# Kernel tuning notes

Measured on AMD Instinct MI355X. Metric: run time of the kernel, lower is better.

The kernel has to match this reference:

```python
import jax, jax.numpy as jnp
import numpy as np

DIM = 768
NUM_HEADS = 12
HEAD_DIM = DIM // NUM_HEADS
H = W = 64
RANK = 4
LORA_SCALING = 1.0 / RANK  # lora_alpha(=1) / r


def setup_inputs() -> dict:
    key = jax.random.key(0)
    ks = jax.random.split(key, 11)
    s = 0.02
    return {
        "x": jax.random.normal(ks[0], (1, H, W, DIM), dtype=jnp.float32),
        "W_qkv": jax.random.normal(ks[1], (3 * DIM, DIM), dtype=jnp.float32) * s,
        "b_qkv": jax.random.normal(ks[2], (3 * DIM,), dtype=jnp.float32) * s,
        "A_q": jax.random.normal(ks[3], (RANK, DIM), dtype=jnp.float32) * s,
        "B_q": jax.random.normal(ks[4], (DIM, RANK), dtype=jnp.float32) * s,
        "A_v": jax.random.normal(ks[5], (RANK, DIM), dtype=jnp.float32) * s,
        "B_v": jax.random.normal(ks[6], (DIM, RANK), dtype=jnp.float32) * s,
        "rel_h": jax.random.normal(ks[7], (2 * H - 1, HEAD_DIM), dtype=jnp.float32) * s,
        "rel_w": jax.random.normal(ks[8], (2 * W - 1, HEAD_DIM), dtype=jnp.float32) * s,
        "W_proj": jax.random.normal(ks[9], (DIM, DIM), dtype=jnp.float32) * s,
        "b_proj": jax.random.normal(ks[10], (DIM,), dtype=jnp.float32) * s,
    }


def _get_rel_pos(size, rel_pos):
    # q_size == k_size == size; relative coords indexed into (2*size-1, head_dim)
    coords = jnp.arange(size)[:, None] - jnp.arange(size)[None, :] + (size - 1)
    return rel_pos[coords]  # (size, size, head_dim)


def reference(x, W_qkv, b_qkv, A_q, B_q, A_v, B_v, rel_h, rel_w, W_proj, b_proj):
    B, h, w, dim = x.shape
    nh, hd = NUM_HEADS, HEAD_DIM
    scale = hd ** -0.5
    n = h * w
    xf = x.reshape(B, n, dim)

    # LoRA-merged QKV: base linear + low-rank deltas on q and v thirds only
    qkv = xf @ W_qkv.T + b_qkv  # (B, n, 3*dim)
    dq = ((xf @ A_q.T) @ B_q.T) * LORA_SCALING
    dv = ((xf @ A_v.T) @ B_v.T) * LORA_SCALING
    qkv = qkv.at[..., :dim].add(dq).at[..., 2 * dim:].add(dv)

    qkv = qkv.reshape(B, n, 3, nh, hd).transpose(2, 0, 3, 1, 4).reshape(3, B * nh, n, hd)
    q, k, v = qkv[0], qkv[1], qkv[2]  # each (B*nh, n, hd)

    attn = (q * scale) @ jnp.swapaxes(k, -2, -1)  # (B*nh, n, n)

    # decomposed relative position bias (SAM style)
    Rh = _get_rel_pos(h, rel_h)  # (h, h, hd)
    Rw = _get_rel_pos(w, rel_w)  # (w, w, hd)
    r_q = q.reshape(B * nh, h, w, hd)
    bias_h = jnp.einsum("bhwc,hkc->bhwk", r_q, Rh)  # (B*nh, h, w, h)
    bias_w = jnp.einsum("bhwc,wkc->bhwk", r_q, Rw)  # (B*nh, h, w, w)
    attn = (attn.reshape(B * nh, h, w, h, w)
            + bias_h[:, :, :, :, None]
            + bias_w[:, :, :, None, :]).reshape(B * nh, n, n)

    attn = jax.nn.softmax(attn, axis=-1)
    out = (attn @ v).reshape(B, nh, h, w, hd).transpose(0, 2, 3, 1, 4).reshape(B, h, w, dim)
    return out @ W_proj.T + b_proj
```

## Files before the change

### kernel.cpp

```cpp
#include <hip/hip_runtime.h>

#define NTOK 4096
#define DIMD 768
#define NHD  12
#define HDD  64

typedef float  f32x4  __attribute__((ext_vector_type(4)));
typedef float  f32x16 __attribute__((ext_vector_type(16)));
typedef short  s16x8  __attribute__((ext_vector_type(8)));

#define MFMA16(a, b, c) __builtin_amdgcn_mfma_f32_16x16x32_bf16(a, b, c, 0, 0, 0)
#define MFMA32(a, b, c) __builtin_amdgcn_mfma_f32_32x32x16_bf16(a, b, c, 0, 0, 0)

__device__ inline short f2b(float f) {
  unsigned u = __float_as_uint(f);
  u += 0x7FFFu + ((u >> 16) & 1u);
  return (short)(u >> 16);
}
__device__ inline float b2f(short s) {
  return __uint_as_float(((unsigned)(unsigned short)s) << 16);
}
__device__ inline void gl_lds16(const short* g, short* l) {
  __builtin_amdgcn_global_load_lds(
      (const __attribute__((address_space(1))) unsigned int*)g,
      (__attribute__((address_space(3))) unsigned int*)l, 16, 0, 0);
}


#define N_WQ  1769472
#define N_WP  589824
__global__ __launch_bounds__(256)
void k_conv(const float* __restrict__ wq, const float* __restrict__ wp,
            short* __restrict__ wqb, short* __restrict__ wpb) {
  long e = (long)(blockIdx.x * 256 + threadIdx.x) * 4;
  const float* src; short* dst;
  if (e < N_WQ) { src = wq + e; dst = wqb + e; }
  else { src = wp + (e - N_WQ); dst = wpb + (e - N_WQ); }
  float4 v = *(const float4*)src;
  short4 b; b.x = f2b(v.x); b.y = f2b(v.y); b.z = f2b(v.z); b.w = f2b(v.w);
  *(short4*)dst = b;
}

__global__ __launch_bounds__(64)
void k_lora(const float* __restrict__ x, const float* __restrict__ Aq,
            const float* __restrict__ Av, float* __restrict__ xaq,
            float* __restrict__ xav, short* __restrict__ xb) {
  const int i = blockIdx.x;
  const int l = threadIdx.x;
  float xv[12];
#pragma unroll
  for (int k = 0; k < 12; ++k) xv[k] = x[i * DIMD + l + 64 * k];
#pragma unroll
  for (int k = 0; k < 12; ++k) xb[i * DIMD + l + 64 * k] = f2b(xv[k]);
#pragma unroll
  for (int o = 0; o < 8; ++o) {
    const float* A = (o < 4) ? (Aq + o * DIMD) : (Av + (o - 4) * DIMD);
    float acc = 0.f;
#pragma unroll
    for (int k = 0; k < 12; ++k) acc = fmaf(xv[k], A[l + 64 * k], acc);
#pragma unroll
    for (int off = 32; off; off >>= 1) acc += __shfl_xor(acc, off, 64);
    if (l == o) {
      if (o < 4) xaq[i * 4 + o] = acc;
      else       xav[i * 4 + (o - 4)] = acc;
    }
  }
}

__global__ __launch_bounds__(256)
void k_qkv(const short* __restrict__ xb, const short* __restrict__ wb,
           const float* __restrict__ bqkv, const float* __restrict__ Bq,
           const float* __restrict__ Bv, const float* __restrict__ xaq,
           const float* __restrict__ xav, short* __restrict__ qkvb) {
  const int j0 = blockIdx.x * 128;
  const int i0 = blockIdx.y * 128;
  __shared__ short As[128 * 32];
  __shared__ short Bs[128 * 32];
  const int t = threadIdx.x, lane = t & 63, w = t >> 6;
  const int l15 = lane & 15, quad = lane >> 4;
  const int wm = w >> 1, wn = w & 1;

  f32x4 acc[4][4];
#pragma unroll
  for (int a = 0; a < 4; ++a)
#pragma unroll
    for (int b = 0; b < 4; ++b) acc[a][b] = (f32x4){0.f, 0.f, 0.f, 0.f};

  for (int kk = 0; kk < DIMD; kk += 32) {
    __syncthreads();
#pragma unroll
    for (int rep = 0; rep < 2; ++rep) {
      int c = rep * 256 + w * 64 + lane;
      gl_lds16(xb + (size_t)(i0 + (c >> 2)) * DIMD + kk + (c & 3) * 8,
               &As[(rep * 256 + w * 64) * 8]);
      gl_lds16(wb + (size_t)(j0 + (c >> 2)) * DIMD + kk + (c & 3) * 8,
               &Bs[(rep * 256 + w * 64) * 8]);
    }
    __syncthreads();
    s16x8 af[4], bf[4];
#pragma unroll
    for (int mt = 0; mt < 4; ++mt)
      af[mt] = *(const s16x8*)&As[(wm * 64 + mt * 16 + l15) * 32 + quad * 8];
#pragma unroll
    for (int nt = 0; nt < 4; ++nt)
      bf[nt] = *(const s16x8*)&Bs[(wn * 64 + nt * 16 + l15) * 32 + quad * 8];
#pragma unroll
    for (int mt = 0; mt < 4; ++mt)
#pragma unroll
      for (int nt = 0; nt < 4; ++nt)
        acc[mt][nt] = MFMA16(af[mt], bf[nt], acc[mt][nt]);
  }

  const int which = j0 / DIMD;
  float bj[4]; int jj[4], head[4], dd[4];
#pragma unroll
  for (int nt = 0; nt < 4; ++nt) {
    int j = j0 + wn * 64 + nt * 16 + l15;
    bj[nt] = bqkv[j];
    jj[nt] = j - which * DIMD;
    head[nt] = jj[nt] >> 6;
    dd[nt] = jj[nt] & 63;
  }
#pragma unroll
  for (int mt = 0; mt < 4; ++mt)
#pragma unroll
    for (int r = 0; r < 4; ++r) {
      const int i = i0 + wm * 64 + mt * 16 + quad * 4 + r;
      float aq0 = 0, aq1 = 0, aq2 = 0, aq3 = 0;
      if (which == 0) {
        const float* a = xaq + i * 4;
        aq0 = a[0]; aq1 = a[1]; aq2 = a[2]; aq3 = a[3];
      } else if (which == 2) {
        const float* a = xav + i * 4;
        aq0 = a[0]; aq1 = a[1]; aq2 = a[2]; aq3 = a[3];
      }
#pragma unroll
      for (int nt = 0; nt < 4; ++nt) {
        float v = acc[mt][nt][r] + bj[nt];
        if (which == 0) {
          const float* B = Bq + jj[nt] * 4;
          v += 0.25f * (aq0 * B[0] + aq1 * B[1] + aq2 * B[2] + aq3 * B[3]);
        } else if (which == 2) {
          const float* B = Bv + jj[nt] * 4;
          v += 0.25f * (aq0 * B[0] + aq1 * B[1] + aq2 * B[2] + aq3 * B[3]);
        }
        qkvb[(((size_t)which * NHD + head[nt]) * NTOK + i) * HDD + dd[nt]] = f2b(v);
      }
    }
}

__global__ __launch_bounds__(256)
void k_vt(const short* __restrict__ qkvb, short* __restrict__ vtb) {
  const int head = blockIdx.y;
  const int n0 = blockIdx.x * 64;
  const short* vg = qkvb + ((size_t)(2 * NHD + head)) * NTOK * HDD;
  __shared__ short T[64][68];
  const int t = threadIdx.x;
#pragma unroll
  for (int rp = 0; rp < 4; ++rp) {
    int f = t + 256 * rp;
    int n = f >> 4, c4 = (f & 15) * 4;
    *(short4*)&T[n][c4] = *(const short4*)&vg[(size_t)(n0 + n) * HDD + c4];
  }
  __syncthreads();
#pragma unroll
  for (int rp = 0; rp < 4; ++rp) {
    int f = t + 256 * rp;
    int d = f >> 4, n4 = (f & 15) * 4;
    short4 o;
    o.x = T[n4 + 0][d]; o.y = T[n4 + 1][d];
    o.z = T[n4 + 2][d]; o.w = T[n4 + 3][d];
    *(short4*)&vtb[((size_t)head * HDD + d) * NTOK + n0 + n4] = o;
  }
}

__global__ __launch_bounds__(256)
void k_attn3(const short* __restrict__ qkvb, const short* __restrict__ vtb,
             const float* __restrict__ relh, const float* __restrict__ relw,
             short* __restrict__ attnb) {
  const int head = blockIdx.y;
  const int hq = blockIdx.x;
  const int n0 = hq * 64;

  __shared__ short sm[17664];
  short* Ks   = sm;
  short* Vt   = sm + 4608;
  short* bHb  = sm + 9216;
  short* tbuf = sm + 13312;
  float* psb  = (float*)(sm + 17536);
  float* obuf = (float*)sm;

  const short* qg  = qkvb + (size_t)(0 * NHD + head) * NTOK * HDD;
  const short* kg  = qkvb + (size_t)(1 * NHD + head) * NTOK * HDD;
  const short* vtg = vtb + (size_t)head * HDD * NTOK;

  const int t = threadIdx.x;
  const int w = t >> 6, lane = t & 63;
  const int l31 = lane & 31, h = lane >> 5;
  const int kh = w >> 1, qh = w & 1;
  const int q = qh * 32 + l31;

  const int sa0 = t >> 3, sc0 = (t & 7) * 8, sa1 = sa0 + 32;

  s16x8 kr0 = *(const s16x8*)&kg[(size_t)sa0 * HDD + sc0];
  s16x8 kr1 = *(const s16x8*)&kg[(size_t)sa1 * HDD + sc0];
  s16x8 vr0 = *(const s16x8*)&vtg[(size_t)sa0 * NTOK + sc0];
  s16x8 vr1 = *(const s16x8*)&vtg[(size_t)sa1 * NTOK + sc0];

  s16x8 qb[4];
#pragma unroll
  for (int s = 0; s < 4; ++s)
    qb[s] = *(const s16x8*)&qg[(size_t)(n0 + q) * HDD + s * 16 + 8 * h];

#pragma unroll
  for (int rp = 0; rp < 4; ++rp) {
    int f = t + 256 * rp;
    int d = f >> 3, c = (f & 7) * 8;
    float4 v0 = make_float4(0, 0, 0, 0), v1 = v0;
    if (d < 127) {
      const float* s_ = relw + (size_t)d * HDD + c;
      v0 = *(const float4*)s_; v1 = *(const float4*)(s_ + 4);
    }
    short4 b0, b1;
    b0.x = f2b(v0.x); b0.y = f2b(v0.y); b0.z = f2b(v0.z); b0.w = f2b(v0.w);
    b1.x = f2b(v1.x); b1.y = f2b(v1.y); b1.z = f2b(v1.z); b1.w = f2b(v1.w);
    *(short4*)&sm[d * 72 + c] = b0;
    *(short4*)&sm[d * 72 + c + 4] = b1;
  }
  __syncthreads();

  f32x16 mc0 = (f32x16)(0.f), mc1 = (f32x16)(0.f);
#pragma unroll
  for (int s = 0; s < 4; ++s) {
    s16x8 a0 = *(const s16x8*)&sm[((kh * 2) * 32 + l31) * 72 + s * 16 + 8 * h];
    s16x8 a1 = *(const s16x8*)&sm[((kh * 2 + 1) * 32 + l31) * 72 + s * 16 + 8 * h];
    mc0 = MFMA32(a0, qb[s], mc0);
    mc1 = MFMA32(a1, qb[s], mc1);
  }
  __syncthreads();
#pragma unroll
  for (int reg = 0; reg < 16; ++reg) {
    int dl = (reg & 3) + 8 * (reg >> 2) + 4 * h;
    sm[(kh * 64 + dl) * 64 + q] = f2b(mc0[reg]);
    sm[(kh * 64 + 32 + dl) * 64 + q] = f2b(mc1[reg]);
  }
  __syncthreads();

  float bwl2[16];
#pragma unroll
  for (int reg = 0; reg < 16; ++reg) {
    int kl64 = kh * 32 + (reg & 3) + 8 * (reg >> 2) + 4 * h;
    int dneed = q - kl64 + 63;
    bwl2[reg] = b2f(sm[dneed * 64 + q]) * 1.44269504f;
  }
  __syncthreads();

#pragma unroll
  for (int rp = 0; rp < 2; ++rp) {
    int f = t + 256 * rp;
    int kt = f >> 3, c = (f & 7) * 8;
    const float* s_ = relh + (size_t)(hq + 63 - kt) * HDD + c;
    float4 v0 = *(const float4*)s_, v1 = *(const float4*)(s_ + 4);
    short4 b0, b1;
    b0.x = f2b(v0.x); b0.y = f2b(v0.y); b0.z = f2b(v0.z); b0.w = f2b(v0.w);
    b1.x = f2b(v1.x); b1.y = f2b(v1.y); b1.z = f2b(v1.z); b1.w = f2b(v1.w);
    *(short4*)&Vt[kt * 72 + c] = b0;
    *(short4*)&Vt[kt * 72 + c + 4] = b1;
  }
  __syncthreads();

  f32x16 hc = (f32x16)(0.f);
#pragma unroll
  for (int s = 0; s < 4; ++s) {
    s16x8 a = *(const s16x8*)&Vt[(kh * 32 + l31) * 72 + s * 16 + 8 * h];
    hc = MFMA32(a, qb[s], hc);
  }
#pragma unroll
  for (int reg = 0; reg < 16; ++reg) {
    int ktl = kh * 32 + (reg & 3) + 8 * (reg >> 2) + 4 * h;
    bHb[ktl * 64 + q] = f2b(hc[reg]);
  }

  float ps = 0.f;
  f32x16 oc0 = (f32x16)(0.f), oc1 = (f32x16)(0.f);

  for (int kt = 0; kt < 64; ++kt) {
    __syncthreads();
    *(s16x8*)&Ks[sa0 * 72 + sc0] = kr0;
    *(s16x8*)&Ks[sa1 * 72 + sc0] = kr1;
    *(s16x8*)&Vt[sa0 * 72 + sc0] = vr0;
    *(s16x8*)&Vt[sa1 * 72 + sc0] = vr1;
    __syncthreads();
    if (kt < 63) {
      const int nk = (kt + 1) * 64;
      kr0 = *(const s16x8*)&kg[(size_t)(nk + sa0) * HDD + sc0];
      kr1 = *(const s16x8*)&kg[(size_t)(nk + sa1) * HDD + sc0];
      vr0 = *(const s16x8*)&vtg[(size_t)sa0 * NTOK + nk + sc0];
      vr1 = *(const s16x8*)&vtg[(size_t)sa1 * NTOK + nk + sc0];
    }

    f32x16 sc_ = (f32x16)(0.f);
#pragma unroll
    for (int s = 0; s < 4; ++s) {
      s16x8 a = *(const s16x8*)&Ks[(kh * 32 + l31) * 72 + s * 16 + 8 * h];
      sc_ = MFMA32(a, qb[s], sc_);
    }

    float bhl2 = b2f(bHb[kt * 64 + q]) * 1.44269504f;
    float sv[16];
#pragma unroll
    for (int reg = 0; reg < 16; ++reg)
      sv[reg] = exp2f(fmaf(0.18033688f, sc_[reg], bhl2 + bwl2[reg]));
#pragma unroll
    for (int reg = 0; reg < 16; ++reg) ps += sv[reg];

    unsigned pk[8], sw[8];
#pragma unroll
    for (int i = 0; i < 8; ++i) {
      int rl = 4 * (i >> 1) + 2 * (i & 1);
      unsigned lo = __float_as_uint(sv[rl]) >> 16;
      unsigned hi = __float_as_uint(sv[rl + 1]) & 0xFFFF0000u;
      pk[i] = hi | lo;
    }
#pragma unroll
    for (int i = 0; i < 8; ++i)
      sw[i] = (unsigned)__shfl_xor((int)pk[i], 32, 64);

#pragma unroll
    for (int s2 = 0; s2 < 2; ++s2) {
      union { unsigned u[4]; s16x8 v; } B;
      B.u[0] = h ? sw[4 * s2 + 2] : pk[4 * s2 + 0];
      B.u[1] = h ? sw[4 * s2 + 3] : pk[4 * s2 + 1];
      B.u[2] = h ? pk[4 * s2 + 2] : sw[4 * s2 + 0];
      B.u[3] = h ? pk[4 * s2 + 3] : sw[4 * s2 + 1];
      s16x8 a0 = *(const s16x8*)&Vt[l31 * 72 + kh * 32 + s2 * 16 + 8 * h];
      s16x8 a1 = *(const s16x8*)&Vt[(32 + l31) * 72 + kh * 32 + s2 * 16 + 8 * h];
      oc0 = MFMA32(a0, B.v, oc0);
      oc1 = MFMA32(a1, B.v, oc1);
    }
  }

  __syncthreads();
  ps += __shfl_xor(ps, 32, 64);
  if (kh == 1) {
#pragma unroll
    for (int reg = 0; reg < 16; ++reg) {
      int dl = (reg & 3) + 8 * (reg >> 2) + 4 * h;
      obuf[dl * 66 + q] = oc0[reg];
      obuf[(32 + dl) * 66 + q] = oc1[reg];
    }
    if (lane < 32) psb[q] = ps;
  }
  __syncthreads();
  if (kh == 0) {
    float inv = 1.f / (ps + psb[q]);
#pragma unroll
    for (int reg = 0; reg < 16; ++reg) {
      int dl = (reg & 3) + 8 * (reg >> 2) + 4 * h;
      tbuf[dl * 66 + q] = f2b((oc0[reg] + obuf[dl * 66 + q]) * inv);
      tbuf[(32 + dl) * 66 + q] = f2b((oc1[reg] + obuf[(32 + dl) * 66 + q]) * inv);
    }
  }
  __syncthreads();
  {
    int qq = t >> 2, seg = t & 3;
    unsigned wds[8];
#pragma unroll
    for (int m = 0; m < 8; ++m) {
      unsigned lo = (unsigned short)tbuf[(seg * 16 + 2 * m) * 66 + qq];
      unsigned hi = (unsigned short)tbuf[(seg * 16 + 2 * m + 1) * 66 + qq];
      wds[m] = lo | (hi << 16);
    }
    short* dst = attnb + (size_t)(n0 + qq) * DIMD + head * 64 + seg * 16;
    *(int4*)dst = *(int4*)&wds[0];
    *(int4*)(dst + 8) = *(int4*)&wds[4];
  }
}

__global__ __launch_bounds__(256)
void k_proj(const short* __restrict__ ab, const short* __restrict__ wpb,
            const float* __restrict__ bp, float* __restrict__ out) {
  const int j0 = blockIdx.x * 64;
  const int i0 = blockIdx.y * 128;
  __shared__ short As[128 * 32];
  __shared__ short Bs[64 * 32];
  const int t = threadIdx.x, lane = t & 63, w = t >> 6;
  const int l15 = lane & 15, quad = lane >> 4;
  const int wm = w >> 1, wn = w & 1;

  f32x4 acc[4][2];
#pragma unroll
  for (int a = 0; a < 4; ++a)
#pragma unroll
    for (int b = 0; b < 2; ++b) acc[a][b] = (f32x4){0.f, 0.f, 0.f, 0.f};

  for (int kk = 0; kk < DIMD; kk += 32) {
    __syncthreads();
#pragma unroll
    for (int rep = 0; rep < 2; ++rep) {
      int c = rep * 256 + w * 64 + lane;
      gl_lds16(ab + (size_t)(i0 + (c >> 2)) * DIMD + kk + (c & 3) * 8,
               &As[(rep * 256 + w * 64) * 8]);
    }
    {
      gl_lds16(wpb + (size_t)(j0 + ((w * 64 + lane) >> 2)) * DIMD + kk +
                   ((w * 64 + lane) & 3) * 8,
               &Bs[(w * 64) * 8]);
    }
    __syncthreads();
    s16x8 af[4], bf[2];
#pragma unroll
    for (int mt = 0; mt < 4; ++mt)
      af[mt] = *(const s16x8*)&As[(wm * 64 + mt * 16 + l15) * 32 + quad * 8];
#pragma unroll
    for (int nt = 0; nt < 2; ++nt)
      bf[nt] = *(const s16x8*)&Bs[(wn * 32 + nt * 16 + l15) * 32 + quad * 8];
#pragma unroll
    for (int mt = 0; mt < 4; ++mt)
#pragma unroll
      for (int nt = 0; nt < 2; ++nt)
        acc[mt][nt] = MFMA16(af[mt], bf[nt], acc[mt][nt]);
  }

#pragma unroll
  for (int mt = 0; mt < 4; ++mt)
#pragma unroll
    for (int r = 0; r < 4; ++r) {
      const int i = i0 + wm * 64 + mt * 16 + quad * 4 + r;
#pragma unroll
      for (int nt = 0; nt < 2; ++nt) {
        const int j = j0 + wn * 32 + nt * 16 + l15;
        out[(size_t)i * DIMD + j] = acc[mt][nt][r] + bp[j];
      }
    }
}

extern "C" void kernel_launch(void* const* d_in, const int* in_sizes, int n_in,
                              void* d_out, int out_size, void* d_ws, size_t ws_size,
                              hipStream_t stream) {
  (void)in_sizes; (void)n_in; (void)out_size; (void)ws_size;
  const float* x    = (const float*)d_in[0];
  const float* Wqkv = (const float*)d_in[1];
  const float* bqkv = (const float*)d_in[2];
  const float* Aq   = (const float*)d_in[3];
  const float* Bq   = (const float*)d_in[4];
  const float* Av   = (const float*)d_in[5];
  const float* Bv   = (const float*)d_in[6];
  const float* relh = (const float*)d_in[7];
  const float* relw = (const float*)d_in[8];
  const float* Wp   = (const float*)d_in[9];
  const float* bp   = (const float*)d_in[10];
  float* out = (float*)d_out;

  float* ws = (float*)d_ws;
  float* xaq  = ws;
  float* xav  = ws + 16384;
  short* xb    = (short*)(ws + 32768);
  short* wqkvb = (short*)(ws + 1605632);
  short* wpb   = (short*)(ws + 2490368);
  short* qkvb  = (short*)(ws + 2785280);
  short* vtb   = (short*)(ws + 7503872);
  short* attnb = (short*)(ws + 9076736);

  k_conv<<<dim3(2304), dim3(256), 0, stream>>>(Wqkv, Wp, wqkvb, wpb);
  k_lora<<<dim3(NTOK), dim3(64), 0, stream>>>(x, Aq, Av, xaq, xav, xb);
  k_qkv<<<dim3(18, 32), dim3(256), 0, stream>>>(xb, wqkvb, bqkv, Bq, Bv, xaq,
                                                xav, qkvb);
  k_vt<<<dim3(64, NHD), dim3(256), 0, stream>>>(qkvb, vtb);
  k_attn3<<<dim3(64, NHD), dim3(256), 0, stream>>>(qkvb, vtb, relh, relw, attnb);
  k_proj<<<dim3(12, 32), dim3(256), 0, stream>>>(attnb, wpb, bp, out);
}
```

Baseline: 262.7 us.

## Fold LoRA into QKV GEMM K-dim and double-buffer attention K/V via LDS DMA

The LoRA low-rank terms are folded into the QKV GEMM by extending the reduction dimension from 768 to 800. The extra columns hold x·A scaled by 1/4 on the activation side and B on the weight side, which removes the per-element LoRA epilogue and the separate xaq/xav buffers. The attention kernel now streams K and V^T tiles straight into double-buffered, XOR-swizzled LDS with global_load_lds instead of staging them through registers, so there is one barrier per iteration instead of two. Weight conversion is merged into one prep kernel. Costs are about 4% more GEMM work and bf16 rounding of the LoRA factors.

```diff
diff --git a/kernel.cpp b/kernel.cpp
--- a/kernel.cpp
+++ b/kernel.cpp
@@ -4,6 +4,7 @@
 #define DIMD 768
 #define NHD  12
 #define HDD  64
+#define DK   800
 
 typedef float  f32x4  __attribute__((ext_vector_type(4)));
 typedef float  f32x16 __attribute__((ext_vector_type(16)));
@@ -27,31 +28,47 @@
 }
 
 
-#define N_WQ  1769472
-#define N_WP  589824
-__global__ __launch_bounds__(256)
-void k_conv(const float* __restrict__ wq, const float* __restrict__ wp,
-            short* __restrict__ wqb, short* __restrict__ wpb) {
-  long e = (long)(blockIdx.x * 256 + threadIdx.x) * 4;
-  const float* src; short* dst;
-  if (e < N_WQ) { src = wq + e; dst = wqb + e; }
-  else { src = wp + (e - N_WQ); dst = wpb + (e - N_WQ); }
-  float4 v = *(const float4*)src;
-  short4 b; b.x = f2b(v.x); b.y = f2b(v.y); b.z = f2b(v.z); b.w = f2b(v.w);
-  *(short4*)dst = b;
-}
-
 __global__ __launch_bounds__(64)
-void k_lora(const float* __restrict__ x, const float* __restrict__ Aq,
-            const float* __restrict__ Av, float* __restrict__ xaq,
-            float* __restrict__ xav, short* __restrict__ xb) {
+void k_prep_w(const float* __restrict__ Wqkv, const float* __restrict__ Bq,
+              const float* __restrict__ Bv, const float* __restrict__ Wp,
+              short* __restrict__ we, short* __restrict__ wpb) {
+  const int j = blockIdx.x;
+  const int l = threadIdx.x;
+  if (j < 2304) {
+#pragma unroll
+    for (int k = 0; k < 12; ++k)
+      we[(size_t)j * DK + l + 64 * k] = f2b(Wqkv[(size_t)j * DIMD + l + 64 * k]);
+    if (l < 32) {
+      int c = 768 + l;
+      short v = 0;
+      if (l < 4) {
+        if (j < 768) v = f2b(Bq[j * 4 + l]);
+      } else if (l < 8) {
+        if (j >= 1536) v = f2b(Bv[(j - 1536) * 4 + (l - 4)]);
+      }
+      we[(size_t)j * DK + c] = v;
+    }
+  } else {
+    const int jr = j - 2304;
+#pragma unroll
+    for (int k = 0; k < 12; ++k)
+      wpb[(size_t)jr * DIMD + l + 64 * k] =
+          f2b(Wp[(size_t)jr * DIMD + l + 64 * k]);
+  }
+}
+
+__global__ __launch_bounds__(64)
+void k_prep_x(const float* __restrict__ x, const float* __restrict__ Aq,
+              const float* __restrict__ Av, short* __restrict__ xe) {
   const int i = blockIdx.x;
   const int l = threadIdx.x;
   float xv[12];
 #pragma unroll
-  for (int k = 0; k < 12; ++k) xv[k] = x[i * DIMD + l + 64 * k];
-#pragma unroll
-  for (int k = 0; k < 12; ++k) xb[i * DIMD + l + 64 * k] = f2b(xv[k]);
+  for (int k = 0; k < 12; ++k) xv[k] = x[(size_t)i * DIMD + l + 64 * k];
+#pragma unroll
+  for (int k = 0; k < 12; ++k)
+    xe[(size_t)i * DK + l + 64 * k] = f2b(xv[k]);
+  float a8[8];
 #pragma unroll
   for (int o = 0; o < 8; ++o) {
     const float* A = (o < 4) ? (Aq + o * DIMD) : (Av + (o - 4) * DIMD);
@@ -60,18 +77,20 @@
     for (int k = 0; k < 12; ++k) acc = fmaf(xv[k], A[l + 64 * k], acc);
 #pragma unroll
     for (int off = 32; off; off >>= 1) acc += __shfl_xor(acc, off, 64);
-    if (l == o) {
-      if (o < 4) xaq[i * 4 + o] = acc;
-      else       xav[i * 4 + (o - 4)] = acc;
-    }
+    a8[o] = acc;
+  }
+  if (l < 32) {
+    float v = 0.f;
+#pragma unroll
+    for (int o = 0; o < 8; ++o)
+      if (l == o) v = 0.25f * a8[o];
+    xe[(size_t)i * DK + 768 + l] = (l < 8) ? f2b(v) : (short)0;
   }
 }
 
 __global__ __launch_bounds__(256)
-void k_qkv(const short* __restrict__ xb, const short* __restrict__ wb,
-           const float* __restrict__ bqkv, const float* __restrict__ Bq,
-           const float* __restrict__ Bv, const float* __restrict__ xaq,
-           const float* __restrict__ xav, short* __restrict__ qkvb) {
+void k_qkv(const short* __restrict__ xe, const short* __restrict__ we,
+           const float* __restrict__ bqkv, short* __restrict__ qkvb) {
   const int j0 = blockIdx.x * 128;
   const int i0 = blockIdx.y * 128;
   __shared__ short As[128 * 32];
@@ -86,14 +105,14 @@
 #pragma unroll
     for (int b = 0; b < 4; ++b) acc[a][b] = (f32x4){0.f, 0.f, 0.f, 0.f};
 
-  for (int kk = 0; kk < DIMD; kk += 32) {
+  for (int kk = 0; kk < DK; kk += 32) {
     __syncthreads();
 #pragma unroll
     for (int rep = 0; rep < 2; ++rep) {
       int c = rep * 256 + w * 64 + lane;
-      gl_lds16(xb + (size_t)(i0 + (c >> 2)) * DIMD + kk + (c & 3) * 8,
+      gl_lds16(xe + (size_t)(i0 + (c >> 2)) * DK + kk + (c & 3) * 8,
                &As[(rep * 256 + w * 64) * 8]);
-      gl_lds16(wb + (size_t)(j0 + (c >> 2)) * DIMD + kk + (c & 3) * 8,
+      gl_lds16(we + (size_t)(j0 + (c >> 2)) * DK + kk + (c & 3) * 8,
                &Bs[(rep * 256 + w * 64) * 8]);
     }
     __syncthreads();
@@ -112,40 +131,24 @@
   }
 
   const int which = j0 / DIMD;
-  float bj[4]; int jj[4], head[4], dd[4];
+  float bj[4]; int head[4], dd[4];
 #pragma unroll
   for (int nt = 0; nt < 4; ++nt) {
     int j = j0 + wn * 64 + nt * 16 + l15;
     bj[nt] = bqkv[j];
-    jj[nt] = j - which * DIMD;
-    head[nt] = jj[nt] >> 6;
-    dd[nt] = jj[nt] & 63;
+    int jj = j - which * DIMD;
+    head[nt] = jj >> 6;
+    dd[nt] = jj & 63;
   }
 #pragma unroll
   for (int mt = 0; mt < 4; ++mt)
 #pragma unroll
     for (int r = 0; r < 4; ++r) {
       const int i = i0 + wm * 64 + mt * 16 + quad * 4 + r;
-      float aq0 = 0, aq1 = 0, aq2 = 0, aq3 = 0;
-      if (which == 0) {
-        const float* a = xaq + i * 4;
-        aq0 = a[0]; aq1 = a[1]; aq2 = a[2]; aq3 = a[3];
-      } else if (which == 2) {
-        const float* a = xav + i * 4;
-        aq0 = a[0]; aq1 = a[1]; aq2 = a[2]; aq3 = a[3];
-      }
-#pragma unroll
-      for (int nt = 0; nt < 4; ++nt) {
-        float v = acc[mt][nt][r] + bj[nt];
-        if (which == 0) {
-          const float* B = Bq + jj[nt] * 4;
-          v += 0.25f * (aq0 * B[0] + aq1 * B[1] + aq2 * B[2] + aq3 * B[3]);
-        } else if (which == 2) {
-          const float* B = Bv + jj[nt] * 4;
-          v += 0.25f * (aq0 * B[0] + aq1 * B[1] + aq2 * B[2] + aq3 * B[3]);
-        }
-        qkvb[(((size_t)which * NHD + head[nt]) * NTOK + i) * HDD + dd[nt]] = f2b(v);
-      }
+#pragma unroll
+      for (int nt = 0; nt < 4; ++nt)
+        qkvb[(((size_t)which * NHD + head[nt]) * NTOK + i) * HDD + dd[nt]] =
+            f2b(acc[mt][nt][r] + bj[nt]);
     }
 }
 
@@ -175,20 +178,15 @@
 }
 
 __global__ __launch_bounds__(256)
-void k_attn3(const short* __restrict__ qkvb, const short* __restrict__ vtb,
+void k_attn4(const short* __restrict__ qkvb, const short* __restrict__ vtb,
              const float* __restrict__ relh, const float* __restrict__ relw,
              short* __restrict__ attnb) {
   const int head = blockIdx.y;
   const int hq = blockIdx.x;
   const int n0 = hq * 64;
 
-  __shared__ short sm[17664];
-  short* Ks   = sm;
-  short* Vt   = sm + 4608;
-  short* bHb  = sm + 9216;
-  short* tbuf = sm + 13312;
-  float* psb  = (float*)(sm + 17536);
-  float* obuf = (float*)sm;
+  __shared__ short sm[20480];
+  short* smb = sm;
 
   const short* qg  = qkvb + (size_t)(0 * NHD + head) * NTOK * HDD;
   const short* kg  = qkvb + (size_t)(1 * NHD + head) * NTOK * HDD;
@@ -200,12 +198,13 @@
   const int kh = w >> 1, qh = w & 1;
   const int q = qh * 32 + l31;
 
-  const int sa0 = t >> 3, sc0 = (t & 7) * 8, sa1 = sa0 + 32;
-
-  s16x8 kr0 = *(const s16x8*)&kg[(size_t)sa0 * HDD + sc0];
-  s16x8 kr1 = *(const s16x8*)&kg[(size_t)sa1 * HDD + sc0];
-  s16x8 vr0 = *(const s16x8*)&vtg[(size_t)sa0 * NTOK + sc0];
-  s16x8 vr1 = *(const s16x8*)&vtg[(size_t)sa1 * NTOK + sc0];
+  const int slot = w * 64 + lane;
+  const int krow = slot >> 3;
+  const int kcol = ((slot & 7) ^ (krow & 7)) * 8;
+  const short* gK0 = kg + (size_t)krow * HDD + kcol;
+  const short* gK1 = gK0 + 32 * HDD;
+  const short* gV0 = vtg + (size_t)krow * NTOK + kcol;
+  const short* gV1 = gV0 + (size_t)32 * NTOK;
 
   s16x8 qb[4];
 #pragma unroll
@@ -224,16 +223,16 @@
     short4 b0, b1;
     b0.x = f2b(v0.x); b0.y = f2b(v0.y); b0.z = f2b(v0.z); b0.w = f2b(v0.w);
     b1.x = f2b(v1.x); b1.y = f2b(v1.y); b1.z = f2b(v1.z); b1.w = f2b(v1.w);
-    *(short4*)&sm[d * 72 + c] = b0;
-    *(short4*)&sm[d * 72 + c + 4] = b1;
+    *(short4*)&smb[d * 72 + c] = b0;
+    *(short4*)&smb[d * 72 + c + 4] = b1;
   }
   __syncthreads();
 
   f32x16 mc0 = (f32x16)(0.f), mc1 = (f32x16)(0.f);
 #pragma unroll
   for (int s = 0; s < 4; ++s) {
-    s16x8 a0 = *(const s16x8*)&sm[((kh * 2) * 32 + l31) * 72 + s * 16 + 8 * h];
-    s16x8 a1 = *(const s16x8*)&sm[((kh * 2 + 1) * 32 + l31) * 72 + s * 16 + 8 * h];
+    s16x8 a0 = *(const s16x8*)&smb[((kh * 2) * 32 + l31) * 72 + s * 16 + 8 * h];
+    s16x8 a1 = *(const s16x8*)&smb[((kh * 2 + 1) * 32 + l31) * 72 + s * 16 + 8 * h];
     mc0 = MFMA32(a0, qb[s], mc0);
     mc1 = MFMA32(a1, qb[s], mc1);
   }
@@ -241,8 +240,8 @@
 #pragma unroll
   for (int reg = 0; reg < 16; ++reg) {
     int dl = (reg & 3) + 8 * (reg >> 2) + 4 * h;
-    sm[(kh * 64 + dl) * 64 + q] = f2b(mc0[reg]);
-    sm[(kh * 64 + 32 + dl) * 64 + q] = f2b(mc1[reg]);
+    smb[(kh * 64 + dl) * 64 + q] = f2b(mc0[reg]);
+    smb[(kh * 64 + 32 + dl) * 64 + q] = f2b(mc1[reg]);
   }
   __syncthreads();
 
@@ -251,7 +250,7 @@
   for (int reg = 0; reg < 16; ++reg) {
     int kl64 = kh * 32 + (reg & 3) + 8 * (reg >> 2) + 4 * h;
     int dneed = q - kl64 + 63;
-    bwl2[reg] = b2f(sm[dneed * 64 + q]) * 1.44269504f;
+    bwl2[reg] = b2f(smb[dneed * 64 + q]) * 1.44269504f;
   }
   __syncthreads();
 
@@ -264,83 +263,93 @@
     short4 b0, b1;
     b0.x = f2b(v0.x); b0.y = f2b(v0.y); b0.z = f2b(v0.z); b0.w = f2b(v0.w);
     b1.x = f2b(v1.x); b1.y = f2b(v1.y); b1.z = f2b(v1.z); b1.w = f2b(v1.w);
-    *(short4*)&Vt[kt * 72 + c] = b0;
-    *(short4*)&Vt[kt * 72 + c + 4] = b1;
+    *(short4*)&smb[kt * 72 + c] = b0;
+    *(short4*)&smb[kt * 72 + c + 4] = b1;
   }
   __syncthreads();
 
   f32x16 hc = (f32x16)(0.f);
 #pragma unroll
   for (int s = 0; s < 4; ++s) {
-    s16x8 a = *(const s16x8*)&Vt[(kh * 32 + l31) * 72 + s * 16 + 8 * h];
+    s16x8 a = *(const s16x8*)&smb[(kh * 32 + l31) * 72 + s * 16 + 8 * h];
     hc = MFMA32(a, qb[s], hc);
   }
 #pragma unroll
   for (int reg = 0; reg < 16; ++reg) {
     int ktl = kh * 32 + (reg & 3) + 8 * (reg >> 2) + 4 * h;
-    bHb[ktl * 64 + q] = f2b(hc[reg]);
-  }
+    smb[16384 + ktl * 64 + q] = f2b(hc[reg]);
+  }
+  __syncthreads();
+
+  gl_lds16(gK0, smb + 0 + w * 512);
+  gl_lds16(gK1, smb + 2048 + w * 512);
+  gl_lds16(gV0, smb + 8192 + w * 512);
+  gl_lds16(gV1, smb + 8192 + 2048 + w * 512);
+  gK0 += 4096; gK1 += 4096; gV0 += 64; gV1 += 64;
+
+  int baseS[4], baseV[2];
+#pragma unroll
+  for (int s = 0; s < 4; ++s)
+    baseS[s] = (kh * 32 + l31) * 64 + (((2 * s + h) ^ (l31 & 7)) * 8);
+#pragma unroll
+  for (int s2 = 0; s2 < 2; ++s2)
+    baseV[s2] = l31 * 64 + (((kh * 4 + s2 * 2 + h) ^ (l31 & 7)) * 8);
 
   float ps = 0.f;
   f32x16 oc0 = (f32x16)(0.f), oc1 = (f32x16)(0.f);
 
-  for (int kt = 0; kt < 64; ++kt) {
-    __syncthreads();
-    *(s16x8*)&Ks[sa0 * 72 + sc0] = kr0;
-    *(s16x8*)&Ks[sa1 * 72 + sc0] = kr1;
-    *(s16x8*)&Vt[sa0 * 72 + sc0] = vr0;
-    *(s16x8*)&Vt[sa1 * 72 + sc0] = vr1;
-    __syncthreads();
-    if (kt < 63) {
-      const int nk = (kt + 1) * 64;
-      kr0 = *(const s16x8*)&kg[(size_t)(nk + sa0) * HDD + sc0];
-      kr1 = *(const s16x8*)&kg[(size_t)(nk + sa1) * HDD + sc0];
-      vr0 = *(const s16x8*)&vtg[(size_t)sa0 * NTOK + nk + sc0];
-      vr1 = *(const s16x8*)&vtg[(size_t)sa1 * NTOK + nk + sc0];
-    }
-
-    f32x16 sc_ = (f32x16)(0.f);
-#pragma unroll
-    for (int s = 0; s < 4; ++s) {
-      s16x8 a = *(const s16x8*)&Ks[(kh * 32 + l31) * 72 + s * 16 + 8 * h];
-      sc_ = MFMA32(a, qb[s], sc_);
-    }
-
-    float bhl2 = b2f(bHb[kt * 64 + q]) * 1.44269504f;
-    float sv[16];
-#pragma unroll
-    for (int reg = 0; reg < 16; ++reg)
-      sv[reg] = exp2f(fmaf(0.18033688f, sc_[reg], bhl2 + bwl2[reg]));
-#pragma unroll
-    for (int reg = 0; reg < 16; ++reg) ps += sv[reg];
-
-    unsigned pk[8], sw[8];
-#pragma unroll
-    for (int i = 0; i < 8; ++i) {
-      int rl = 4 * (i >> 1) + 2 * (i & 1);
-      unsigned lo = __float_as_uint(sv[rl]) >> 16;
-      unsigned hi = __float_as_uint(sv[rl + 1]) & 0xFFFF0000u;
-      pk[i] = hi | lo;
-    }
-#pragma unroll
-    for (int i = 0; i < 8; ++i)
-      sw[i] = (unsigned)__shfl_xor((int)pk[i], 32, 64);
-
-#pragma unroll
-    for (int s2 = 0; s2 < 2; ++s2) {
-      union { unsigned u[4]; s16x8 v; } B;
-      B.u[0] = h ? sw[4 * s2 + 2] : pk[4 * s2 + 0];
-      B.u[1] = h ? sw[4 * s2 + 3] : pk[4 * s2 + 1];
-      B.u[2] = h ? pk[4 * s2 + 2] : sw[4 * s2 + 0];
-      B.u[3] = h ? pk[4 * s2 + 3] : sw[4 * s2 + 1];
-      s16x8 a0 = *(const s16x8*)&Vt[l31 * 72 + kh * 32 + s2 * 16 + 8 * h];
-      s16x8 a1 = *(const s16x8*)&Vt[(32 + l31) * 72 + kh * 32 + s2 * 16 + 8 * h];
-      oc0 = MFMA32(a0, B.v, oc0);
-      oc1 = MFMA32(a1, B.v, oc1);
-    }
-  }
-
-  __syncthreads();
+#define ATTN_ITER(KT, KSRC, VSRC, KDST, VDST)                                  \
+  {                                                                            \
+    __syncthreads();                                                           \
+    if ((KT) < 63) {                                                           \
+      gl_lds16(gK0, smb + (KDST) + w * 512);                                   \
+      gl_lds16(gK1, smb + (KDST) + 2048 + w * 512);                            \
+      gl_lds16(gV0, smb + (VDST) + w * 512);                                   \
+      gl_lds16(gV1, smb + (VDST) + 2048 + w * 512);                            \
+      gK0 += 4096; gK1 += 4096; gV0 += 64; gV1 += 64;                          \
+    }                                                                          \
+    f32x16 sc_ = (f32x16)(0.f);                                                \
+    _Pragma("unroll") for (int s = 0; s < 4; ++s) {                            \
+      s16x8 a = *(const s16x8*)&smb[(KSRC) + baseS[s]];                        \
+      sc_ = MFMA32(a, qb[s], sc_);                                             \
+    }                                                                          \
+    float bhl2 = b2f(smb[16384 + (KT) * 64 + q]) * 1.44269504f;                \
+    float sv[16];                                                              \
+    _Pragma("unroll") for (int reg = 0; reg < 16; ++reg) {                     \
+      sv[reg] = exp2f(fmaf(0.18033688f, sc_[reg], bhl2 + bwl2[reg]));          \
+      ps += sv[reg];                                                           \
+    }                                                                          \
+    unsigned pk[8], sw[8];                                                     \
+    _Pragma("unroll") for (int i = 0; i < 8; ++i) {                            \
+      int rl = 4 * (i >> 1) + 2 * (i & 1);                                     \
+      pk[i] = __builtin_amdgcn_perm(__float_as_uint(sv[rl + 1]),               \
+                                    __float_as_uint(sv[rl]), 0x07060302u);     \
+    }                                                                          \
+    _Pragma("unroll") for (int i = 0; i < 8; ++i)                              \
+      sw[i] = (unsigned)__shfl_xor((int)pk[i], 32, 64);                        \
+    _Pragma("unroll") for (int s2 = 0; s2 < 2; ++s2) {                         \
+      union { unsigned u[4]; s16x8 v; } B;                                     \
+      B.u[0] = h ? sw[4 * s2 + 2] : pk[4 * s2 + 0];                            \
+      B.u[1] = h ? sw[4 * s2 + 3] : pk[4 * s2 + 1];                            \
+      B.u[2] = h ? pk[4 * s2 + 2] : sw[4 * s2 + 0];                            \
+      B.u[3] = h ? pk[4 * s2 + 3] : sw[4 * s2 + 1];                            \
+      s16x8 a0 = *(const s16x8*)&smb[(VSRC) + baseV[s2]];                      \
+      s16x8 a1 = *(const s16x8*)&smb[(VSRC) + 2048 + baseV[s2]];               \
+      oc0 = MFMA32(a0, B.v, oc0);                                              \
+      oc1 = MFMA32(a1, B.v, oc1);                                              \
+    }                                                                          \
+  }
+
+  for (int k2 = 0; k2 < 32; ++k2) {
+    ATTN_ITER(2 * k2, 0, 8192, 4096, 12288);
+    ATTN_ITER(2 * k2 + 1, 4096, 12288, 0, 8192);
+  }
+#undef ATTN_ITER
+
+  __syncthreads();
+  float* obuf = (float*)smb;
+  float* psb  = (float*)smb + 4224;
+  short* tbuf = smb + 8576;
   ps += __shfl_xor(ps, 32, 64);
   if (kh == 1) {
 #pragma unroll
@@ -453,20 +462,17 @@
   float* out = (float*)d_out;
 
   float* ws = (float*)d_ws;
-  float* xaq  = ws;
-  float* xav  = ws + 16384;
-  short* xb    = (short*)(ws + 32768);
-  short* wqkvb = (short*)(ws + 1605632);
-  short* wpb   = (short*)(ws + 2490368);
-  short* qkvb  = (short*)(ws + 2785280);
-  short* vtb   = (short*)(ws + 7503872);
-  short* attnb = (short*)(ws + 9076736);
-
-  k_conv<<<dim3(2304), dim3(256), 0, stream>>>(Wqkv, Wp, wqkvb, wpb);
-  k_lora<<<dim3(NTOK), dim3(64), 0, stream>>>(x, Aq, Av, xaq, xav, xb);
-  k_qkv<<<dim3(18, 32), dim3(256), 0, stream>>>(xb, wqkvb, bqkv, Bq, Bv, xaq,
-                                                xav, qkvb);
+  short* xe    = (short*)(ws);
+  short* we    = (short*)(ws + 1638400);
+  short* wpb   = (short*)(ws + 2560000);
+  short* qkvb  = (short*)(ws + 2854912);
+  short* vtb   = (short*)(ws + 7573504);
+  short* attnb = (short*)(ws + 9146368);
+
+  k_prep_w<<<dim3(3072), dim3(64), 0, stream>>>(Wqkv, Bq, Bv, Wp, we, wpb);
+  k_prep_x<<<dim3(NTOK), dim3(64), 0, stream>>>(x, Aq, Av, xe);
+  k_qkv<<<dim3(18, 32), dim3(256), 0, stream>>>(xe, we, bqkv, qkvb);
   k_vt<<<dim3(64, NHD), dim3(256), 0, stream>>>(qkvb, vtb);
-  k_attn3<<<dim3(64, NHD), dim3(256), 0, stream>>>(qkvb, vtb, relh, relw, attnb);
+  k_attn4<<<dim3(64, NHD), dim3(256), 0, stream>>>(qkvb, vtb, relh, relw, attnb);
   k_proj<<<dim3(12, 32), dim3(256), 0, stream>>>(attnb, wpb, bp, out);
 }
```

New measurement: 276.4 us. 5.2% more time.
